# Kernel tuning notes

Measured on AMD Instinct MI355X. Metric: run time of the kernel, lower is better.

The kernel has to match this reference:

```python
import jax, jax.numpy as jnp
import numpy as np

N, K, P, C, H, E, Q, G = 50000, 8, 512, 64, 128, 1600000, 500000, 64

def _gelu(x):
    return jax.nn.gelu(x, approximate=False)  # torch F.gelu default = exact erf

def _mlp(x, Wi, bi, Wh, bh, Wo, bo, Wp=None, bp=None):
    # MLP: lin_in -> gelu -> hid -> (proj skip if in>hidden) -> skip+gelu -> lin_out
    skip = x if Wp is None else x @ Wp.T + bp
    h = _gelu(x @ Wi.T + bi)
    h = h @ Wh.T + bh
    return (skip + _gelu(h)) @ Wo.T + bo

def _sage(x, src, dst, Wl, bl, Wr, n):
    # PyG SAGEConv: mean-aggregate source features at dst, then lin_l(agg)+lin_r(x)
    s = jax.ops.segment_sum(x[src], dst, num_segments=n)
    cnt = jax.ops.segment_sum(jnp.ones((src.shape[0], 1), x.dtype), dst, num_segments=n)
    agg = s / jnp.maximum(cnt, 1.0)
    return agg @ Wl.T + bl + x @ Wr.T

def setup_inputs():
    key = jax.random.key(0)
    ks = iter(jax.random.split(key, 64))
    def lin(o, i):
        return (jax.random.normal(next(ks), (o, i), jnp.float32) / np.sqrt(i)).astype(jnp.float32)
    def bias(o):
        return jnp.zeros((o,), jnp.float32)
    inp = {}
    inp["x"] = jax.random.normal(next(ks), (N, K, P), jnp.float32)
    inp["batch"] = jnp.sort(jax.random.randint(next(ks), (N,), 0, G))
    inp["edge_index"] = jax.random.randint(next(ks), (2, E), 0, N)
    inp["src_idx"] = jax.random.randint(next(ks), (Q,), 0, N)
    inp["dst_idx"] = jax.random.randint(next(ks), (Q,), 0, N)
    # Embedder.mlp : MLP(P, P, H) with proj (P > H)
    inp.update(em_in_W=lin(H, P), em_in_b=bias(H), em_hid_W=lin(H, H), em_hid_b=bias(H),
               em_out_W=lin(P, H), em_out_b=bias(P), em_proj_W=lin(H, P), em_proj_b=bias(H))
    # Embedder.rho : MLP(P, C, H) with proj
    inp.update(rho_in_W=lin(H, P), rho_in_b=bias(H), rho_hid_W=lin(H, H), rho_hid_b=bias(H),
               rho_out_W=lin(C, H), rho_out_b=bias(C), rho_proj_W=lin(H, P), rho_proj_b=bias(H))
    for i in (1, 2, 3):
        inp[f"c{i}_ll_W"] = lin(C, C); inp[f"c{i}_ll_b"] = bias(C); inp[f"c{i}_lr_W"] = lin(C, C)
    # head MLP(3C, 2C, 2C) with proj (3C > 2C)
    inp.update(h1_in_W=lin(H, 3 * C), h1_in_b=bias(H), h1_hid_W=lin(H, H), h1_hid_b=bias(H),
               h1_out_W=lin(2 * C, H), h1_out_b=bias(2 * C), h1_proj_W=lin(H, 3 * C), h1_proj_b=bias(H))
    # head MLP(2C, 1, 2C), no proj
    inp.update(h2_in_W=lin(H, 2 * C), h2_in_b=bias(H), h2_hid_W=lin(H, H), h2_hid_b=bias(H),
               h2_out_W=lin(1, H), h2_out_b=bias(1))
    return inp

def reference(x, batch, edge_index, src_idx, dst_idx,
              em_in_W, em_in_b, em_hid_W, em_hid_b, em_out_W, em_out_b, em_proj_W, em_proj_b,
              rho_in_W, rho_in_b, rho_hid_W, rho_hid_b, rho_out_W, rho_out_b, rho_proj_W, rho_proj_b,
              c1_ll_W, c1_ll_b, c1_lr_W, c2_ll_W, c2_ll_b, c2_lr_W, c3_ll_W, c3_ll_b, c3_lr_W,
              h1_in_W, h1_in_b, h1_hid_W, h1_hid_b, h1_out_W, h1_out_b, h1_proj_W, h1_proj_b,
              h2_in_W, h2_in_b, h2_hid_W, h2_hid_b, h2_out_W, h2_out_b):
    n = x.shape[0]
    # Embedder: per-point MLP, gelu, sum over point-set dim, then rho (dropout = eval identity)
    h = _gelu(_mlp(x, em_in_W, em_in_b, em_hid_W, em_hid_b, em_out_W, em_out_b, em_proj_W, em_proj_b))
    z = _mlp(h.sum(-2), rho_in_W, rho_in_b, rho_hid_W, rho_hid_b, rho_out_W, rho_out_b, rho_proj_W, rho_proj_b)
    src, dst = edge_index[0], edge_index[1]
    z = z + _gelu(_sage(z, src, dst, c1_ll_W, c1_ll_b, c1_lr_W, n))
    z = z + _gelu(_sage(z, src, dst, c2_ll_W, c2_ll_b, c2_lr_W, n))
    z = z + _gelu(_sage(z, src, dst, c3_ll_W, c3_ll_b, c3_lr_W, n))
    node_embeddings = z
    # global_max_pool keyed by batch id, broadcast back via gather
    graph_emb = jax.ops.segment_max(z, batch, num_segments=G)
    ge = graph_emb[batch[src_idx]]  # == graph_emb[batch][src_idx]
    se, de = z[src_idx], z[dst_idx]
    xy = jnp.concatenate([se, de, ge], axis=-1)
    yx = jnp.concatenate([de, se, ge], axis=-1)
    def head(q):
        t = jax.nn.relu(_mlp(q, h1_in_W, h1_in_b, h1_hid_W, h1_hid_b, h1_out_W, h1_out_b, h1_proj_W, h1_proj_b))
        return _mlp(t, h2_in_W, h2_in_b, h2_hid_W, h2_hid_b, h2_out_W, h2_out_b)
    return (node_embeddings, (head(xy), head(yx)), xy)
```

## Files before the change

### kernel.cpp

```cpp
#include <hip/hip_runtime.h>

typedef unsigned short US;
typedef unsigned int   UI;
typedef short  short8 __attribute__((ext_vector_type(8)));
typedef US     u16x8  __attribute__((ext_vector_type(8)));
typedef float  f32x4  __attribute__((ext_vector_type(4)));

#define DEVI __device__ __forceinline__

DEVI float bf2f(US u){ UI i = ((UI)u) << 16; float f; __builtin_memcpy(&f, &i, 4); return f; }
DEVI US f2bf(float x){ UI i; __builtin_memcpy(&i, &x, 4); UI r = (i + 0x7FFFu + ((i >> 16) & 1u)) >> 16; return (US)r; }
DEVI float gelu_f(float x){
    float x2 = x * x;
    float m  = x * fmaf(x2, -0.1029432f, -2.3022052f);
    float e  = __builtin_amdgcn_exp2f(m);
    return x * __builtin_amdgcn_rcpf(1.0f + e);
}
DEVI UI encf(float f){ UI u; __builtin_memcpy(&u, &f, 4); return (u & 0x80000000u) ? ~u : (u | 0x80000000u); }
DEVI float decf(UI u){ UI b = (u & 0x80000000u) ? (u ^ 0x80000000u) : ~u; float f; __builtin_memcpy(&f, &b, 4); return f; }
DEVI int swz(int r, int c, int ld){ int i = r * ld + c; return i ^ ((r & 7) << 3); }

DEVI UI pkbf(float a, float b){ UI u; asm("v_cvt_pk_bf16_f32 %0, %1, %2" : "=v"(u) : "v"(a), "v"(b)); return u; }
DEVI void st4(US* T, int row, int col, float v0, float v1, float v2, float v3){
    uint2 p; p.x = pkbf(v0, v1); p.y = pkbf(v2, v3);
    *(uint2*)&T[swz(row, col, 256)] = p;
}
DEVI void ld4(const US* T, int row, int col, float& v0, float& v1, float& v2, float& v3){
    uint2 q = *(const uint2*)&T[swz(row, col, 256)];
    v0 = bf2f((US)(q.x & 0xffff)); v1 = bf2f((US)(q.x >> 16));
    v2 = bf2f((US)(q.y & 0xffff)); v3 = bf2f((US)(q.y >> 16));
}

enum : int { O_EmW1 = 0, O_EmWh = 131072, O_EmWo = 147456, O_RhoW1 = 212992,
             O_RhoWh = 344064, O_RhoWo = 360448, O_Cat1 = 368640, O_Cat2 = 376832,
             O_Cat3 = 385024, O_H1W1 = 393216, O_H1Wh = 442368, O_H1Wo = 458752,
             O_H2W1 = 475136, O_H2Wh = 491520, W_TOTAL = 507904 };

template<int NT, int NKC, int NTHR, bool SWAP = false>
DEVI void stageWD(const US* __restrict__ Wg, int Kw, const US* __restrict__ A, int lda,
                  int ab0, int ab1, int ab2, int arow0, US* Wb, int tid, f32x4 (&acc)[NT])
{
    const int lane = tid & 63;
    const int wc = (tid >> 6) & 1;
    constexpr int SLAB = NT * 32 * 64;
    #pragma unroll
    for (int n = 0; n < NT; ++n) acc[n] = (f32x4){0.f, 0.f, 0.f, 0.f};
    constexpr int J = (NT * 256) / NTHR;
    u16x8 wreg[J];
    #pragma unroll
    for (int j = 0; j < J; ++j) {
        const int c = tid + NTHR * j;
        wreg[j] = *(const u16x8*)(Wg + (size_t)(c >> 3) * Kw + (c & 7) * 8);
    }
    #pragma unroll
    for (int j = 0; j < J; ++j) {
        const int c = tid + NTHR * j;
        *(u16x8*)&Wb[swz(c >> 3, (c & 7) * 8, 64)] = wreg[j];
    }
    #pragma unroll
    for (int kc = 0; kc < NKC; ++kc) {
        __syncthreads();
        if (kc + 1 < NKC) {
            #pragma unroll
            for (int j = 0; j < J; ++j) {
                const int c = tid + NTHR * j;
                wreg[j] = *(const u16x8*)(Wg + (size_t)(c >> 3) * Kw + (kc + 1) * 64 + (c & 7) * 8);
            }
        }
        const int ab = (kc == 0) ? ab0 : ((kc == 1) ? ab1 : ab2);
        const int bufr = (kc & 1) * SLAB;
        #pragma unroll
        for (int sub = 0; sub < 2; ++sub) {
            const int kk = sub * 32 + ((lane >> 4) << 3);
            short8 a = *(const short8*)&A[swz(arow0 + (lane & 15), ab + kk, lda)];
            #pragma unroll
            for (int n = 0; n < NT; ++n) {
                short8 b = *(const short8*)&Wb[bufr + swz(wc * (NT * 16) + n * 16 + (lane & 15), kk, 64)];
                if (SWAP) acc[n] = __builtin_amdgcn_mfma_f32_16x16x32_bf16(b, a, acc[n], 0, 0, 0);
                else      acc[n] = __builtin_amdgcn_mfma_f32_16x16x32_bf16(a, b, acc[n], 0, 0, 0);
            }
        }
        if (kc + 1 < NKC) {
            const int bufw = ((kc + 1) & 1) * SLAB;
            #pragma unroll
            for (int j = 0; j < J; ++j) {
                const int c = tid + NTHR * j;
                *(u16x8*)&Wb[bufw + swz(c >> 3, (c & 7) * 8, 64)] = wreg[j];
            }
        }
    }
    __syncthreads();
}

template<int NT, int NTN, int NKC, int NTHR, bool LAST, bool SWAP = true>
DEVI void stageWC(const US* __restrict__ Wg, int Kw, const US* __restrict__ nextWg, int nKw,
                  const US* __restrict__ A, int lda, int ab0, int ab1, int ab2, int arow0,
                  US* Wb, int off0, int off1, int wrN, int tid, f32x4 (&acc)[NT])
{
    const int lane = tid & 63;
    const int wc = (tid >> 6) & 1;
    #pragma unroll
    for (int n = 0; n < NT; ++n) acc[n] = (f32x4){0.f, 0.f, 0.f, 0.f};
    constexpr int J  = (NT  * 256) / NTHR;
    constexpr int JN = (NTN * 256) / NTHR;
    constexpr int JM = (J > JN) ? J : JN;
    u16x8 wreg[JM];
    #pragma unroll
    for (int kc = 0; kc < NKC; ++kc) {
        __syncthreads();
        if (kc + 1 < NKC) {
            #pragma unroll
            for (int j = 0; j < J; ++j) {
                const int c = tid + NTHR * j;
                wreg[j] = *(const u16x8*)(Wg + (size_t)(c >> 3) * Kw + (kc + 1) * 64 + (c & 7) * 8);
            }
        } else if (!LAST) {
            #pragma unroll
            for (int j = 0; j < JN; ++j) {
                const int c = tid + NTHR * j;
                wreg[j] = *(const u16x8*)(nextWg + (size_t)(c >> 3) * nKw + (c & 7) * 8);
            }
        }
        const int ab = (kc == 0) ? ab0 : ((kc == 1) ? ab1 : ab2);
        const int rd = (kc & 1) ? off1 : off0;
        #pragma unroll
        for (int sub = 0; sub < 2; ++sub) {
            const int kk = sub * 32 + ((lane >> 4) << 3);
            short8 a = *(const short8*)&A[swz(arow0 + (lane & 15), ab + kk, lda)];
            #pragma unroll
            for (int n = 0; n < NT; ++n) {
                short8 b = *(const short8*)&Wb[rd + swz(wc * (NT * 16) + n * 16 + (lane & 15), kk, 64)];
                if (SWAP) acc[n] = __builtin_amdgcn_mfma_f32_16x16x32_bf16(b, a, acc[n], 0, 0, 0);
                else      acc[n] = __builtin_amdgcn_mfma_f32_16x16x32_bf16(a, b, acc[n], 0, 0, 0);
            }
        }
        if (kc + 1 < NKC) {
            const int wr_ = (kc & 1) ? off0 : off1;
            #pragma unroll
            for (int j = 0; j < J; ++j) {
                const int c = tid + NTHR * j;
                *(u16x8*)&Wb[wr_ + swz(c >> 3, (c & 7) * 8, 64)] = wreg[j];
            }
        } else if (!LAST) {
            #pragma unroll
            for (int j = 0; j < JN; ++j) {
                const int c = tid + NTHR * j;
                *(u16x8*)&Wb[wrN + swz(c >> 3, (c & 7) * 8, 64)] = wreg[j];
            }
        }
    }
    __syncthreads();
}

template<int NT, int NTHR>
DEVI void preloadW(const US* __restrict__ Wg, int Kw, US* Wb, int off, int tid)
{
    constexpr int J = (NT * 256) / NTHR;
    #pragma unroll
    for (int j = 0; j < J; ++j) {
        const int c = tid + NTHR * j;
        u16x8 v = *(const u16x8*)(Wg + (size_t)(c >> 3) * Kw + (c & 7) * 8);
        *(u16x8*)&Wb[off + swz(c >> 3, (c & 7) * 8, 64)] = v;
    }
}

__global__ __launch_bounds__(1024, 4)
void embed_fused(const float* __restrict__ x, const US* __restrict__ WB,
                 const float* __restrict__ b_in, const float* __restrict__ b_proj,
                 const float* __restrict__ b_hid, const float* __restrict__ b_out,
                 US* __restrict__ Ss)
{
    __shared__ __align__(16) US T1[128 * 256];
    __shared__ __align__(16) US Wb[2 * 16384];
    const int tid = threadIdx.x, lane = tid & 63, w = tid >> 6;
    const int wr = w >> 1, wc = w & 1;
    const int h = lane >> 4;
    const int grow0 = blockIdx.x * 128;
    const int rowT = wr * 16 + (lane & 15);

    {
        f32x4 acc[8];
        #pragma unroll
        for (int n = 0; n < 8; ++n) acc[n] = (f32x4){0.f, 0.f, 0.f, 0.f};
        const float* xp = x + (size_t)(grow0 + rowT) * 512 + h * 8;
        float4 pA0, pA1, pA2, pA3, pB0, pB1, pB2, pB3;
        u16x8 wreg[2];
        auto loadW = [&](int kc) {
            #pragma unroll
            for (int j = 0; j < 2; ++j) {
                const int c = tid + 1024 * j;
                wreg[j] = *(const u16x8*)(WB + O_EmW1 + (size_t)(c >> 3) * 512 + kc * 64 + (c & 7) * 8);
            }
        };
        auto writeW = [&](int buf) {
            #pragma unroll
            for (int j = 0; j < 2; ++j) {
                const int c = tid + 1024 * j;
                *(u16x8*)&Wb[buf * 16384 + swz(c >> 3, (c & 7) * 8, 64)] = wreg[j];
            }
        };
        pA0 = *(const float4*)(xp +   0); pA1 = *(const float4*)(xp +   4);
        pA2 = *(const float4*)(xp +  32); pA3 = *(const float4*)(xp +  36);
        loadW(0);
        pB0 = *(const float4*)(xp +  64); pB1 = *(const float4*)(xp +  68);
        pB2 = *(const float4*)(xp +  96); pB3 = *(const float4*)(xp + 100);
        writeW(0);
        #pragma unroll
        for (int k2 = 0; k2 < 4; ++k2) {
            const int kce = 2 * k2, kco = 2 * k2 + 1;
            __syncthreads();
            short8 a0, a1;
            {
                uint4 q;
                q.x = pkbf(pA0.x, pA0.y); q.y = pkbf(pA0.z, pA0.w);
                q.z = pkbf(pA1.x, pA1.y); q.w = pkbf(pA1.z, pA1.w);
                __builtin_memcpy(&a0, &q, 16);
                q.x = pkbf(pA2.x, pA2.y); q.y = pkbf(pA2.z, pA2.w);
                q.z = pkbf(pA3.x, pA3.y); q.w = pkbf(pA3.z, pA3.w);
                __builtin_memcpy(&a1, &q, 16);
            }
            if (kce + 2 < 8) {
                pA0 = *(const float4*)(xp + (kce + 2) * 64);
                pA1 = *(const float4*)(xp + (kce + 2) * 64 + 4);
                pA2 = *(const float4*)(xp + (kce + 2) * 64 + 32);
                pA3 = *(const float4*)(xp + (kce + 2) * 64 + 36);
            }
            loadW(kco);
            #pragma unroll
            for (int n = 0; n < 8; ++n) {
                short8 b = *(const short8*)&Wb[swz(wc * 128 + n * 16 + (lane & 15), h * 8, 64)];
                acc[n] = __builtin_amdgcn_mfma_f32_16x16x32_bf16(b, a0, acc[n], 0, 0, 0);
            }
            #pragma unroll
            for (int n = 0; n < 8; ++n) {
                short8 b = *(const short8*)&Wb[swz(wc * 128 + n * 16 + (lane & 15), 32 + h * 8, 64)];
                acc[n] = __builtin_amdgcn_mfma_f32_16x16x32_bf16(b, a1, acc[n], 0, 0, 0);
            }
            writeW(1);
            __syncthreads();
            {
                uint4 q;
                q.x = pkbf(pB0.x, pB0.y); q.y = pkbf(pB0.z, pB0.w);
                q.z = pkbf(pB1.x, pB1.y); q.w = pkbf(pB1.z, pB1.w);
                __builtin_memcpy(&a0, &q, 16);
                q.x = pkbf(pB2.x, pB2.y); q.y = pkbf(pB2.z, pB2.w);
                q.z = pkbf(pB3.x, pB3.y); q.w = pkbf(pB3.z, pB3.w);
                __builtin_memcpy(&a1, &q, 16);
            }
            if (kco + 2 < 8) {
                pB0 = *(const float4*)(xp + (kco + 2) * 64);
                pB1 = *(const float4*)(xp + (kco + 2) * 64 + 4);
                pB2 = *(const float4*)(xp + (kco + 2) * 64 + 32);
                pB3 = *(const float4*)(xp + (kco + 2) * 64 + 36);
            }
            u16x8 nx;
            if (kco < 7) loadW(kco + 1);
            else         nx = *(const u16x8*)(WB + O_EmWh + (size_t)(tid >> 3) * 128 + (tid & 7) * 8);
            #pragma unroll
            for (int n = 0; n < 8; ++n) {
                short8 b = *(const short8*)&Wb[16384 + swz(wc * 128 + n * 16 + (lane & 15), h * 8, 64)];
                acc[n] = __builtin_amdgcn_mfma_f32_16x16x32_bf16(b, a0, acc[n], 0, 0, 0);
            }
            #pragma unroll
            for (int n = 0; n < 8; ++n) {
                short8 b = *(const short8*)&Wb[16384 + swz(wc * 128 + n * 16 + (lane & 15), 32 + h * 8, 64)];
                acc[n] = __builtin_amdgcn_mfma_f32_16x16x32_bf16(b, a1, acc[n], 0, 0, 0);
            }
            if (kco < 7) writeW(0);
            else         *(u16x8*)&Wb[swz(tid >> 3, (tid & 7) * 8, 64)] = nx;
        }
        #pragma unroll
        for (int n = 0; n < 8; ++n) {
            const int col = wc * 128 + n * 16 + h * 4;
            float4 bv = (col < 128) ? *(const float4*)&b_in[col]
                                    : *(const float4*)&b_proj[col - 128];
            float v0 = acc[n][0] + bv.x, v1 = acc[n][1] + bv.y;
            float v2 = acc[n][2] + bv.z, v3 = acc[n][3] + bv.w;
            if (col < 128) { v0 = gelu_f(v0); v1 = gelu_f(v1); v2 = gelu_f(v2); v3 = gelu_f(v3); }
            st4(T1, rowT, col, v0, v1, v2, v3);
        }
    }
    {
        f32x4 acc[4];
        stageWC<4, 8, 2, 1024, false, true>(WB + O_EmWh, 128, WB + O_EmWo, 128,
                                            T1, 256, 0, 64, 0, wr * 16,
                                            Wb, 0, 8192, 16384, tid, acc);
        #pragma unroll
        for (int n = 0; n < 4; ++n) {
            const int col = wc * 64 + n * 16 + h * 4;
            float4 bv = *(const float4*)&b_hid[col];
            float s0, s1, s2, s3;
            ld4(T1, rowT, 128 + col, s0, s1, s2, s3);
            st4(T1, rowT, col,
                gelu_f(acc[n][0] + bv.x) + s0, gelu_f(acc[n][1] + bv.y) + s1,
                gelu_f(acc[n][2] + bv.z) + s2, gelu_f(acc[n][3] + bv.w) + s3);
        }
    }
    {
        f32x4 acc[8];
        stageWC<8, 8, 2, 1024, false, false>(WB + O_EmWo, 128, WB + O_EmWo + (size_t)256 * 128, 128,
                                             T1, 256, 0, 64, 0, wr * 16,
                                             Wb, 16384, 0, 16384, tid, acc);
        #pragma unroll
        for (int n = 0; n < 8; ++n) {
            const int col = wc * 128 + n * 16 + (lane & 15);
            const float bv = b_out[col];
            float s = 0.f;
            #pragma unroll
            for (int r = 0; r < 4; ++r) s += gelu_f(acc[n][r] + bv);
            s += __shfl_xor(s, 16);
            if (((lane >> 4) & 1) == 0) {
                const int node = (grow0 >> 3) + wr * 2 + (lane >> 5);
                Ss[(size_t)node * 512 + col] = f2bf(s);
            }
        }
    }
    {
        f32x4 acc[8];
        stageWC<8, 8, 2, 1024, true, false>(WB + O_EmWo + (size_t)256 * 128, 128, (const US*)nullptr, 0,
                                            T1, 256, 0, 64, 0, wr * 16,
                                            Wb, 16384, 0, 16384, tid, acc);
        #pragma unroll
        for (int n = 0; n < 8; ++n) {
            const int col = wc * 128 + n * 16 + (lane & 15);
            const float bv = b_out[256 + col];
            float s = 0.f;
            #pragma unroll
            for (int r = 0; r < 4; ++r) s += gelu_f(acc[n][r] + bv);
            s += __shfl_xor(s, 16);
            if (((lane >> 4) & 1) == 0) {
                const int node = (grow0 >> 3) + wr * 2 + (lane >> 5);
                Ss[(size_t)node * 512 + 256 + col] = f2bf(s);
            }
        }
    }
}

__global__ __launch_bounds__(512, 2)
void rho_fused(const US* __restrict__ Ss, const US* __restrict__ WB,
               const float* __restrict__ b_in, const float* __restrict__ b_proj,
               const float* __restrict__ b_hid, const float* __restrict__ b_out,
               US* __restrict__ zo, int N)
{
    __shared__ __align__(16) US T1[64 * 256];
    __shared__ __align__(16) US Wb[256 * 64];
    const int tid = threadIdx.x, lane = tid & 63, w = tid >> 6;
    const int wr = w >> 1, wc = w & 1;
    const int h = lane >> 4;
    const int grow0 = blockIdx.x * 64;
    const int rowT = wr * 16 + (lane & 15);

    {
        f32x4 acc[8];
        #pragma unroll
        for (int n = 0; n < 8; ++n) acc[n] = (f32x4){0.f, 0.f, 0.f, 0.f};
        int arow = grow0 + rowT; if (arow >= N) arow = N - 1;
        const US* sp = Ss + (size_t)arow * 512 + h * 8;
        u16x8 a0r, a1r, wreg[4];
        auto loadA = [&](int kc) {
            a0r = *(const u16x8*)(sp + kc * 64);
            a1r = *(const u16x8*)(sp + kc * 64 + 32);
        };
        auto loadW = [&](int kc) {
            #pragma unroll
            for (int j = 0; j < 4; ++j) {
                const int c = tid + 512 * j;
                wreg[j] = *(const u16x8*)(WB + O_RhoW1 + (size_t)(c >> 3) * 512 + kc * 64 + (c & 7) * 8);
            }
        };
        loadA(0); loadW(0);
        for (int kc = 0; kc < 8; ++kc) {
            __syncthreads();
            #pragma unroll
            for (int j = 0; j < 4; ++j) {
                const int c = tid + 512 * j;
                *(u16x8*)&Wb[swz(c >> 3, (c & 7) * 8, 64)] = wreg[j];
            }
            __syncthreads();
            if (kc < 7) loadW(kc + 1);
            short8 a0, a1;
            __builtin_memcpy(&a0, &a0r, 16);
            __builtin_memcpy(&a1, &a1r, 16);
            #pragma unroll
            for (int n = 0; n < 8; ++n) {
                short8 b = *(const short8*)&Wb[swz(wc * 128 + n * 16 + (lane & 15), h * 8, 64)];
                acc[n] = __builtin_amdgcn_mfma_f32_16x16x32_bf16(b, a0, acc[n], 0, 0, 0);
            }
            #pragma unroll
            for (int n = 0; n < 8; ++n) {
                short8 b = *(const short8*)&Wb[swz(wc * 128 + n * 16 + (lane & 15), 32 + h * 8, 64)];
                acc[n] = __builtin_amdgcn_mfma_f32_16x16x32_bf16(b, a1, acc[n], 0, 0, 0);
            }
            if (kc < 7) loadA(kc + 1);
        }
        __syncthreads();
        #pragma unroll
        for (int n = 0; n < 8; ++n) {
            const int col = wc * 128 + n * 16 + h * 4;
            float4 bv = (col < 128) ? *(const float4*)&b_in[col]
                                    : *(const float4*)&b_proj[col - 128];
            float v0 = acc[n][0] + bv.x, v1 = acc[n][1] + bv.y;
            float v2 = acc[n][2] + bv.z, v3 = acc[n][3] + bv.w;
            if (col < 128) { v0 = gelu_f(v0); v1 = gelu_f(v1); v2 = gelu_f(v2); v3 = gelu_f(v3); }
            st4(T1, rowT, col, v0, v1, v2, v3);
        }
    }
    {
        f32x4 acc[4];
        stageWD<4, 2, 512, true>(WB + O_RhoWh, 128, T1, 256, 0, 64, 0, wr * 16, Wb, tid, acc);
        #pragma unroll
        for (int n = 0; n < 4; ++n) {
            const int col = wc * 64 + n * 16 + h * 4;
            float4 bv = *(const float4*)&b_hid[col];
            float s0, s1, s2, s3;
            ld4(T1, rowT, 128 + col, s0, s1, s2, s3);
            st4(T1, rowT, col,
                gelu_f(acc[n][0] + bv.x) + s0, gelu_f(acc[n][1] + bv.y) + s1,
                gelu_f(acc[n][2] + bv.z) + s2, gelu_f(acc[n][3] + bv.w) + s3);
        }
    }
    {
        f32x4 acc[2];
        stageWD<2, 2, 512>(WB + O_RhoWo, 128, T1, 256, 0, 64, 0, wr * 16, Wb, tid, acc);
        #pragma unroll
        for (int n = 0; n < 2; ++n) {
            const int col = wc * 32 + n * 16 + (lane & 15);
            const float bv = b_out[col];
            #pragma unroll
            for (int r = 0; r < 4; ++r) {
                const int node = grow0 + wr * 16 + h * 4 + r;
                if (node < N) zo[(size_t)node * 64 + col] = f2bf(acc[n][r] + bv);
            }
        }
    }
}

__global__ __launch_bounds__(1024, 4)
void head_fused(const int* __restrict__ srcq, const int* __restrict__ dstq,
                const int* __restrict__ batch, const US* __restrict__ z,
                const US* __restrict__ geb, const US* __restrict__ WB,
                const float* __restrict__ b1_in, const float* __restrict__ b1_proj,
                const float* __restrict__ b1_hid, const float* __restrict__ b1_out,
                const float* __restrict__ b2_in, const float* __restrict__ b2_hid,
                const float* __restrict__ w2_out, const float* __restrict__ b2_out,
                float* __restrict__ outH, float* __restrict__ outXY, int Q)
{
    __shared__ __align__(16) US A0[64 * 192];
    __shared__ __align__(16) US T1[128 * 256];
    __shared__ __align__(16) US Wb[2 * 16384];
    __shared__ float wout_s[128];
    const int tid = threadIdx.x, lane = tid & 63, w = tid >> 6;
    const int wr = w >> 1, wc = w & 1;
    const int q0 = blockIdx.x * 64;
    const int s1a = (wr < 4) ? 0 : 64;
    const int s1b = (wr < 4) ? 64 : 0;
    const int arowS1 = (wr & 3) * 16;
    const int rowS1 = (wr >> 2) * 64 + arowS1 + (lane & 15);
    const int rowT  = wr * 16 + (lane & 15);

    preloadW<8, 1024>(WB + O_H1W1, 192, Wb, 0, tid);

    {
        if (tid < 512) {
            const int r = tid >> 3, hh = tid & 7;
            const int q = q0 + r;
            const int qc = (q < Q) ? q : (Q - 1);
            const int s = srcq[qc], d = dstq[qc];
            const int g = batch[s];
            *(u16x8*)&A0[swz(r, hh * 8, 192)]       = *(const u16x8*)(z + (size_t)s * 64 + hh * 8);
            *(u16x8*)&A0[swz(r, 64 + hh * 8, 192)]  = *(const u16x8*)(z + (size_t)d * 64 + hh * 8);
            *(u16x8*)&A0[swz(r, 128 + hh * 8, 192)] = *(const u16x8*)(geb + (size_t)g * 64 + hh * 8);
        }
        if (tid < 128) wout_s[tid] = w2_out[tid];
    }
    __syncthreads();
    {
        const int row = tid >> 4;
        const int qu  = tid & 15;
        #pragma unroll
        for (int jj = 0; jj < 3; ++jj) {
            const int c4 = (jj * 16 + qu) * 4;
            if (q0 + row < Q) {
                const US* p = &A0[swz(row, c4, 192)];
                float4 o;
                o.x = bf2f(p[0]); o.y = bf2f(p[1]); o.z = bf2f(p[2]); o.w = bf2f(p[3]);
                *(float4*)&outXY[(size_t)(q0 + row) * 192 + c4] = o;
            }
        }
    }
    {
        f32x4 acc8[8];
        stageWC<8, 4, 3, 1024, false>(WB + O_H1W1, 192, WB + O_H1Wh, 128,
                                      A0, 192, s1a, s1b, 128, arowS1,
                                      Wb, 0, 16384, 16384, tid, acc8);
        #pragma unroll
        for (int n = 0; n < 8; ++n) {
            const int col = wc * 128 + n * 16 + ((lane >> 4) << 2);
            float4 bv = (col < 128) ? *(const float4*)&b1_in[col]
                                    : *(const float4*)&b1_proj[col - 128];
            float v0 = acc8[n][0] + bv.x, v1 = acc8[n][1] + bv.y;
            float v2 = acc8[n][2] + bv.z, v3 = acc8[n][3] + bv.w;
            if (col < 128) { v0 = gelu_f(v0); v1 = gelu_f(v1); v2 = gelu_f(v2); v3 = gelu_f(v3); }
            st4(T1, rowS1, col, v0, v1, v2, v3);
        }
    }
    f32x4 acc[4];
    stageWC<4, 4, 2, 1024, false>(WB + O_H1Wh, 128, WB + O_H1Wo, 128,
                                  T1, 256, 0, 64, 0, wr * 16,
                                  Wb, 16384, 24576, 16384, tid, acc);
    #pragma unroll
    for (int n = 0; n < 4; ++n) {
        const int col = wc * 64 + n * 16 + ((lane >> 4) << 2);
        float4 bv = *(const float4*)&b1_hid[col];
        float s0, s1, s2, s3;
        ld4(T1, rowT, 128 + col, s0, s1, s2, s3);
        st4(T1, rowT, col,
            gelu_f(acc[n][0] + bv.x) + s0, gelu_f(acc[n][1] + bv.y) + s1,
            gelu_f(acc[n][2] + bv.z) + s2, gelu_f(acc[n][3] + bv.w) + s3);
    }
    stageWC<4, 4, 2, 1024, false>(WB + O_H1Wo, 128, WB + O_H2W1, 128,
                                  T1, 256, 0, 64, 0, wr * 16,
                                  Wb, 16384, 24576, 16384, tid, acc);
    #pragma unroll
    for (int n = 0; n < 4; ++n) {
        const int col = wc * 64 + n * 16 + ((lane >> 4) << 2);
        float4 bv = *(const float4*)&b1_out[col];
        st4(T1, rowT, 128 + col,
            fmaxf(acc[n][0] + bv.x, 0.f), fmaxf(acc[n][1] + bv.y, 0.f),
            fmaxf(acc[n][2] + bv.z, 0.f), fmaxf(acc[n][3] + bv.w, 0.f));
    }
    stageWC<4, 4, 2, 1024, false>(WB + O_H2W1, 128, WB + O_H2Wh, 128,
                                  T1, 256, 128, 192, 0, wr * 16,
                                  Wb, 16384, 24576, 16384, tid, acc);
    #pragma unroll
    for (int n = 0; n < 4; ++n) {
        const int col = wc * 64 + n * 16 + ((lane >> 4) << 2);
        float4 bv = *(const float4*)&b2_in[col];
        st4(T1, rowT, col,
            gelu_f(acc[n][0] + bv.x), gelu_f(acc[n][1] + bv.y),
            gelu_f(acc[n][2] + bv.z), gelu_f(acc[n][3] + bv.w));
    }
    stageWC<4, 4, 2, 1024, true>(WB + O_H2Wh, 128, (const US*)nullptr, 0,
                                 T1, 256, 0, 64, 0, wr * 16,
                                 Wb, 16384, 24576, 16384, tid, acc);
    #pragma unroll
    for (int n = 0; n < 4; ++n) {
        const int col = wc * 64 + n * 16 + ((lane >> 4) << 2);
        float4 bv = *(const float4*)&b2_hid[col];
        float t0, t1, t2, t3;
        ld4(T1, rowT, 128 + col, t0, t1, t2, t3);
        st4(T1, rowT, col,
            gelu_f(acc[n][0] + bv.x) + t0, gelu_f(acc[n][1] + bv.y) + t1,
            gelu_f(acc[n][2] + bv.z) + t2, gelu_f(acc[n][3] + bv.w) + t3);
    }
    __syncthreads();
    {
        const int r = tid >> 3, hh = tid & 7;
        float a = 0.f;
        u16x8 v0 = *(const u16x8*)&T1[swz(r, hh * 16, 256)];
        u16x8 v1 = *(const u16x8*)&T1[swz(r, hh * 16 + 8, 256)];
        #pragma unroll
        for (int e = 0; e < 8; ++e) {
            a += bf2f(v0[e]) * wout_s[hh * 16 + e];
            a += bf2f(v1[e]) * wout_s[hh * 16 + 8 + e];
        }
        a += __shfl_xor(a, 4);
        a += __shfl_xor(a, 2);
        a += __shfl_xor(a, 1);
        const int q = q0 + (r & 63);
        if ((lane & 7) == 0 && q < Q) outH[(size_t)(r >> 6) * Q + q] = a + b2_out[0];
    }
}

__global__ __launch_bounds__(256, 2)
void sage_gemm(const US* __restrict__ zin, const US* __restrict__ agg,
               const US* __restrict__ Wc, const float* __restrict__ bias,
               US* __restrict__ zout, float* __restrict__ fout, int N)
{
    __shared__ __align__(16) US As[128 * 128];
    __shared__ __align__(16) US Ws[64 * 128];
    const int tid = threadIdx.x, lane = tid & 63, w = tid >> 6;
    const int grow0 = blockIdx.x * 128;
    {
        const int r = tid >> 1, hh = tid & 1;
        int row = grow0 + r; if (row >= N) row = N - 1;
        const US* src = hh ? (zin + (size_t)row * 64) : (agg + (size_t)row * 64);
        #pragma unroll
        for (int j = 0; j < 8; ++j)
            *(u16x8*)&As[swz(r, hh * 64 + 8 * j, 128)] = *(const u16x8*)(src + 8 * j);
    }
    #pragma unroll
    for (int j = 0; j < 4; ++j) {
        const int c = tid + 256 * j;
        *(u16x8*)&Ws[swz(c >> 4, (c & 15) * 8, 128)] =
            *(const u16x8*)(Wc + (size_t)(c >> 4) * 128 + (c & 15) * 8);
    }
    __syncthreads();
    const int rbw = w * 32;
    f32x4 acc[2][4];
    #pragma unroll
    for (int m = 0; m < 2; ++m)
        #pragma unroll
        for (int n = 0; n < 4; ++n) acc[m][n] = (f32x4){0.f, 0.f, 0.f, 0.f};
    #pragma unroll
    for (int kc = 0; kc < 2; ++kc)
        #pragma unroll
        for (int sub = 0; sub < 2; ++sub) {
            const int kk = kc * 64 + sub * 32 + ((lane >> 4) << 3);
            short8 a[2], b[4];
            #pragma unroll
            for (int m = 0; m < 2; ++m) a[m] = *(const short8*)&As[swz(rbw + m * 16 + (lane & 15), kk, 128)];
            #pragma unroll
            for (int n = 0; n < 4; ++n) b[n] = *(const short8*)&Ws[swz(n * 16 + (lane & 15), kk, 128)];
            #pragma unroll
            for (int m = 0; m < 2; ++m)
                #pragma unroll
                for (int n = 0; n < 4; ++n)
                    acc[m][n] = __builtin_amdgcn_mfma_f32_16x16x32_bf16(a[m], b[n], acc[m][n], 0, 0, 0);
        }
    #pragma unroll
    for (int m = 0; m < 2; ++m) {
        const int row0 = rbw + m * 16 + ((lane >> 4) << 2);
        #pragma unroll
        for (int n = 0; n < 4; ++n) {
            const int col = n * 16 + (lane & 15);
            const float bv = bias[col];
            #pragma unroll
            for (int r = 0; r < 4; ++r) {
                const int node = grow0 + row0 + r;
                if (node < N) {
                    const float v = gelu_f(acc[m][n][r] + bv) + bf2f(zin[(size_t)node * 64 + col]);
                    const US bb = f2bf(v);
                    zout[(size_t)node * 64 + col] = bb;
                    if (fout) fout[(size_t)node * 64 + col] = bf2f(bb);
                }
            }
        }
    }
}

struct WSeg { const float* src; int dst; int n; int rl; int ldd; };
struct WPrm { WSeg s[20]; };

__global__ void prep_w(WPrm p, US* __restrict__ wb)
{
    WSeg sg = p.s[blockIdx.x];
    for (int i = threadIdx.x; i < sg.n; i += 256) {
        const int idx = sg.dst + (i / sg.rl) * sg.ldd + (i % sg.rl);
        wb[idx] = f2bf(sg.src[i]);
    }
}

__global__ void count_k(const int* __restrict__ dst, int* __restrict__ cnt, int E)
{
    int e = blockIdx.x * 256 + threadIdx.x;
    if (e < E) atomicAdd(&cnt[dst[e]], 1);
}

__global__ void scan_csr(const int* __restrict__ cnt, int n, int* __restrict__ indp, int* __restrict__ curs)
{
    __shared__ int wsum[16];
    __shared__ int carry_s;
    const int tid = threadIdx.x, lane = tid & 63, w = tid >> 6;
    if (tid == 0) carry_s = 0;
    __syncthreads();
    for (int base = 0; base < n; base += 1024) {
        const int i = base + tid;
        const int v = (i < n) ? cnt[i] : 0;
        int s = v;
        #pragma unroll
        for (int o = 1; o < 64; o <<= 1) { int t = __shfl_up(s, o); if (lane >= o) s += t; }
        if (lane == 63) wsum[w] = s;
        __syncthreads();
        if (w == 0 && lane < 16) {
            int ws2 = wsum[lane];
            #pragma unroll
            for (int o = 1; o < 16; o <<= 1) { int t = __shfl_up(ws2, o); if (lane >= o) ws2 += t; }
            wsum[lane] = ws2;
        }
        __syncthreads();
        const int carry = carry_s;
        const int woff  = (w == 0) ? 0 : wsum[w - 1];
        if (i < n) { const int excl = carry + woff + s - v; indp[i] = excl; curs[i] = excl; }
        __syncthreads();
        if (tid == 0) carry_s = carry + wsum[15];
        __syncthreads();
    }
    if (threadIdx.x == 0) indp[n] = carry_s;
}

__global__ void fill_k(const int* __restrict__ src, const int* __restrict__ dst,
                       int* __restrict__ curs, int* __restrict__ esrc, int E)
{
    int e = blockIdx.x * 256 + threadIdx.x;
    if (e < E) { int p = atomicAdd(&curs[dst[e]], 1); esrc[p] = src[e]; }
}

__global__ void sage_agg(const US* __restrict__ z, const int* __restrict__ indp,
                         const int* __restrict__ esrc, US* __restrict__ agg, int n)
{
    const int w = blockIdx.x * 4 + (threadIdx.x >> 6);
    const int lane = threadIdx.x & 63;
    if (w >= n) return;
    const int beg = indp[w], end = indp[w + 1];
    float acc = 0.f;
    int j = beg;
    for (; j + 4 <= end; j += 4) {
        const int s0 = esrc[j], s1 = esrc[j + 1], s2 = esrc[j + 2], s3 = esrc[j + 3];
        const float v0 = bf2f(z[(size_t)s0 * 64 + lane]);
        const float v1 = bf2f(z[(size_t)s1 * 64 + lane]);
        const float v2 = bf2f(z[(size_t)s2 * 64 + lane]);
        const float v3 = bf2f(z[(size_t)s3 * 64 + lane]);
        acc += (v0 + v1) + (v2 + v3);
    }
    for (; j < end; ++j) acc += bf2f(z[(size_t)esrc[j] * 64 + lane]);
    const float d = (float)(end - beg);
    agg[(size_t)w * 64 + lane] = f2bf(acc / fmaxf(d, 1.0f));
}

__global__ void segmax_k(const US* __restrict__ z, const int* __restrict__ batch,
                         UI* __restrict__ enc, int n, int per)
{
    const int w = blockIdx.x * 4 + (threadIdx.x >> 6);
    const int lane = threadIdx.x & 63;
    const int start = w * per;
    if (start >= n) return;
    const int end = (start + per < n) ? start + per : n;
    int g = batch[start];
    float m = -3.0e38f;
    for (int i = start; i < end; ++i) {
        const int b = batch[i];
        if (b != g) { atomicMax(&enc[(size_t)g * 64 + lane], encf(m)); g = b; m = -3.0e38f; }
        m = fmaxf(m, bf2f(z[(size_t)i * 64 + lane]));
    }
    atomicMax(&enc[(size_t)g * 64 + lane], encf(m));
}

__global__ void decode_ge(const UI* __restrict__ enc, US* __restrict__ geb)
{
    const int i = blockIdx.x * 256 + threadIdx.x;
    if (i < 4096) geb[i] = f2bf(decf(enc[i]));
}

extern "C" void kernel_launch(void* const* d_in, const int* in_sizes, int n_in,
                              void* d_out, int out_size, void* d_ws, size_t ws_size,
                              hipStream_t stream)
{
    (void)in_sizes; (void)n_in; (void)out_size; (void)ws_size;

    const float* x      = (const float*)d_in[0];
    const int*   batch  = (const int*)d_in[1];
    const int*   eidx   = (const int*)d_in[2];
    const int*   srcq   = (const int*)d_in[3];
    const int*   dstq   = (const int*)d_in[4];
    const float* em_in_b   = (const float*)d_in[6];
    const float* em_hid_b  = (const float*)d_in[8];
    const float* em_out_b  = (const float*)d_in[10];
    const float* em_proj_b = (const float*)d_in[12];
    const float* rho_in_b  = (const float*)d_in[14];
    const float* rho_hid_b = (const float*)d_in[16];
    const float* rho_out_b = (const float*)d_in[18];
    const float* rho_proj_b= (const float*)d_in[20];
    const float* c_ll_W[3] = {(const float*)d_in[21], (const float*)d_in[24], (const float*)d_in[27]};
    const float* c_ll_b[3] = {(const float*)d_in[22], (const float*)d_in[25], (const float*)d_in[28]};
    const float* c_lr_W[3] = {(const float*)d_in[23], (const float*)d_in[26], (const float*)d_in[29]};
    const float* h1_in_b   = (const float*)d_in[31];
    const float* h1_hid_b  = (const float*)d_in[33];
    const float* h1_out_b  = (const float*)d_in[35];
    const float* h1_proj_b = (const float*)d_in[37];
    const float* h2_in_b   = (const float*)d_in[39];
    const float* h2_hid_b  = (const float*)d_in[41];
    const float* h2_out_W  = (const float*)d_in[42];
    const float* h2_out_b  = (const float*)d_in[43];

    const int N = 50000, E = 1600000, Q = 500000;
    float* out = (float*)d_out;

    char* wsb = (char*)d_ws;
    size_t off = 0;
    auto ALLOC = [&](size_t bytes) -> char* {
        char* p = wsb + off; off = (off + bytes + 255) & ~(size_t)255; return p;
    };
    US*  WB   = (US*)ALLOC((size_t)W_TOTAL * 2);
    US*  Ss   = (US*)ALLOC((size_t)N * 512 * 2);
    US*  z0   = (US*)ALLOC((size_t)N * 64 * 2);
    US*  z1   = (US*)ALLOC((size_t)N * 64 * 2);
    US*  aggB = (US*)ALLOC((size_t)N * 64 * 2);
    int* cnt  = (int*)ALLOC((size_t)N * 4);
    int* indp = (int*)ALLOC((size_t)(N + 1) * 4);
    int* curs = (int*)ALLOC((size_t)N * 4);
    int* esrc = (int*)ALLOC((size_t)E * 4);
    UI*  enc  = (UI*)ALLOC(4096 * 4);
    US*  geb  = (US*)ALLOC(4096 * 2);

    const int catOff[3] = {O_Cat1, O_Cat2, O_Cat3};

    WPrm pw; int si = 0;
    auto SEG = [&](const float* s, int o, int n, int rl, int ldd) {
        pw.s[si].src = s; pw.s[si].dst = o; pw.s[si].n = n; pw.s[si].rl = rl; pw.s[si].ldd = ldd; ++si;
    };
    SEG((const float*)d_in[5],  O_EmW1,          65536, 65536, 65536);
    SEG((const float*)d_in[11], O_EmW1 + 65536,  65536, 65536, 65536);
    SEG((const float*)d_in[7],  O_EmWh,          16384, 16384, 16384);
    SEG((const float*)d_in[9],  O_EmWo,          65536, 65536, 65536);
    SEG((const float*)d_in[13], O_RhoW1,         65536, 65536, 65536);
    SEG((const float*)d_in[19], O_RhoW1 + 65536, 65536, 65536, 65536);
    SEG((const float*)d_in[15], O_RhoWh,         16384, 16384, 16384);
    SEG((const float*)d_in[17], O_RhoWo,          8192,  8192,  8192);
    for (int i = 0; i < 3; ++i) {
        SEG(c_ll_W[i], catOff[i],      4096, 64, 128);
        SEG(c_lr_W[i], catOff[i] + 64, 4096, 64, 128);
    }
    SEG((const float*)d_in[30], O_H1W1,          24576, 24576, 24576);
    SEG((const float*)d_in[36], O_H1W1 + 24576,  24576, 24576, 24576);
    SEG((const float*)d_in[32], O_H1Wh,          16384, 16384, 16384);
    SEG((const float*)d_in[34], O_H1Wo,          16384, 16384, 16384);
    SEG((const float*)d_in[38], O_H2W1,          16384, 16384, 16384);
    SEG((const float*)d_in[40], O_H2Wh,          16384, 16384, 16384);
    prep_w<<<dim3(20), dim3(256), 0, stream>>>(pw, WB);

    hipMemsetAsync(cnt, 0, (size_t)N * 4, stream);
    count_k<<<dim3((E + 255) / 256), dim3(256), 0, stream>>>(eidx + E, cnt, E);
    scan_csr<<<dim3(1), dim3(1024), 0, stream>>>(cnt, N, indp, curs);
    fill_k<<<dim3((E + 255) / 256), dim3(256), 0, stream>>>(eidx, eidx + E, curs, esrc, E);

    embed_fused<<<dim3(3125), dim3(1024), 0, stream>>>(x, WB, em_in_b, em_proj_b, em_hid_b, em_out_b, Ss);
    rho_fused<<<dim3((N + 63) / 64), dim3(512), 0, stream>>>(Ss, WB, rho_in_b, rho_proj_b, rho_hid_b, rho_out_b, z0, N);

    US* zin = z0; US* zout = z1;
    for (int ci = 0; ci < 3; ++ci) {
        sage_agg<<<dim3((N + 3) / 4), dim3(256), 0, stream>>>(zin, indp, esrc, aggB, N);
        sage_gemm<<<dim3((N + 127) / 128), dim3(256), 0, stream>>>(
            zin, aggB, WB + catOff[ci], c_ll_b[ci], zout,
            (ci == 2) ? out : (float*)nullptr, N);
        US* t = zin; zin = zout; zout = t;
    }
    US* zf = zin;

    hipMemsetAsync(enc, 0, 4096 * 4, stream);
    segmax_k<<<dim3((N + 511) / 512), dim3(256), 0, stream>>>(zf, batch, enc, N, 128);
    decode_ge<<<dim3(16), dim3(256), 0, stream>>>(enc, geb);

    head_fused<<<dim3((Q + 63) / 64), dim3(1024), 0, stream>>>(
        srcq, dstq, batch, zf, geb, WB,
        h1_in_b, h1_proj_b, h1_hid_b, h1_out_b, h2_in_b, h2_hid_b, h2_out_W, h2_out_b,
        out + (size_t)N * 64, out + (size_t)N * 64 + 2 * (size_t)Q, Q);
}
```

Measured before the change: 1.544 ms.

## Retile MLP stages so each wave computes two row tiles sharing weight fragments

Replaces the per-wave 16-row × wide-column GEMM tiling with a 4×4 warp grid where each wave processes two 16-row tiles (rows r and r+64) over a narrower column slice. Each weight fragment read from LDS now feeds two MFMAs, which roughly halves LDS traffic for the B operand across the embedder tail and head MLP stages. The cost is an extra A-fragment load and doubled accumulators per wave, which raises register pressure under the 1024-thread launch bound.

```diff
diff --git a/kernel.cpp b/kernel.cpp
--- a/kernel.cpp
+++ b/kernel.cpp
@@ -92,17 +92,24 @@
     __syncthreads();
 }
 
-template<int NT, int NTN, int NKC, int NTHR, bool LAST, bool SWAP = true>
-DEVI void stageWC(const US* __restrict__ Wg, int Kw, const US* __restrict__ nextWg, int nKw,
-                  const US* __restrict__ A, int lda, int ab0, int ab1, int ab2, int arow0,
-                  US* Wb, int off0, int off1, int wrN, int tid, f32x4 (&acc)[NT])
+template<int NT, int TOTC, int TOTCN, int NKC, bool LAST, bool SWAP>
+DEVI void stageWC2(const US* __restrict__ Wg, int Kw, const US* __restrict__ nextWg, int nKw,
+                   const US* __restrict__ A, int lda,
+                   int aA0, int aA1, int aA2, int aB0, int aB1, int aB2,
+                   int arowA, int rofB, int colb,
+                   US* Wb, int off0, int off1, int wrN, int tid,
+                   f32x4 (&accA)[NT], f32x4 (&accB)[NT])
 {
     const int lane = tid & 63;
-    const int wc = (tid >> 6) & 1;
-    #pragma unroll
-    for (int n = 0; n < NT; ++n) acc[n] = (f32x4){0.f, 0.f, 0.f, 0.f};
-    constexpr int J  = (NT  * 256) / NTHR;
-    constexpr int JN = (NTN * 256) / NTHR;
+    const int l15 = lane & 15;
+    const int h8 = (lane >> 4) << 3;
+    #pragma unroll
+    for (int n = 0; n < NT; ++n) {
+        accA[n] = (f32x4){0.f, 0.f, 0.f, 0.f};
+        accB[n] = (f32x4){0.f, 0.f, 0.f, 0.f};
+    }
+    constexpr int J  = TOTC  / 128;
+    constexpr int JN = TOTCN / 128;
     constexpr int JM = (J > JN) ? J : JN;
     u16x8 wreg[JM];
     #pragma unroll
@@ -111,40 +118,47 @@
         if (kc + 1 < NKC) {
             #pragma unroll
             for (int j = 0; j < J; ++j) {
-                const int c = tid + NTHR * j;
+                const int c = tid + 1024 * j;
                 wreg[j] = *(const u16x8*)(Wg + (size_t)(c >> 3) * Kw + (kc + 1) * 64 + (c & 7) * 8);
             }
         } else if (!LAST) {
             #pragma unroll
             for (int j = 0; j < JN; ++j) {
-                const int c = tid + NTHR * j;
+                const int c = tid + 1024 * j;
                 wreg[j] = *(const u16x8*)(nextWg + (size_t)(c >> 3) * nKw + (c & 7) * 8);
             }
         }
-        const int ab = (kc == 0) ? ab0 : ((kc == 1) ? ab1 : ab2);
+        const int abA = (kc == 0) ? aA0 : ((kc == 1) ? aA1 : aA2);
+        const int abB = (kc == 0) ? aB0 : ((kc == 1) ? aB1 : aB2);
         const int rd = (kc & 1) ? off1 : off0;
         #pragma unroll
         for (int sub = 0; sub < 2; ++sub) {
-            const int kk = sub * 32 + ((lane >> 4) << 3);
-            short8 a = *(const short8*)&A[swz(arow0 + (lane & 15), ab + kk, lda)];
+            const int kk = sub * 32 + h8;
+            short8 aA = *(const short8*)&A[swz(arowA + l15, abA + kk, lda)];
+            short8 aB = *(const short8*)&A[swz(arowA + rofB + l15, abB + kk, lda)];
             #pragma unroll
             for (int n = 0; n < NT; ++n) {
-                short8 b = *(const short8*)&Wb[rd + swz(wc * (NT * 16) + n * 16 + (lane & 15), kk, 64)];
-                if (SWAP) acc[n] = __builtin_amdgcn_mfma_f32_16x16x32_bf16(b, a, acc[n], 0, 0, 0);
-                else      acc[n] = __builtin_amdgcn_mfma_f32_16x16x32_bf16(a, b, acc[n], 0, 0, 0);
+                short8 b = *(const short8*)&Wb[rd + swz(colb + n * 16 + l15, kk, 64)];
+                if (SWAP) {
+                    accA[n] = __builtin_amdgcn_mfma_f32_16x16x32_bf16(b, aA, accA[n], 0, 0, 0);
+                    accB[n] = __builtin_amdgcn_mfma_f32_16x16x32_bf16(b, aB, accB[n], 0, 0, 0);
+                } else {
+                    accA[n] = __builtin_amdgcn_mfma_f32_16x16x32_bf16(aA, b, accA[n], 0, 0, 0);
+                    accB[n] = __builtin_amdgcn_mfma_f32_16x16x32_bf16(aB, b, accB[n], 0, 0, 0);
+                }
             }
         }
         if (kc + 1 < NKC) {
             const int wr_ = (kc & 1) ? off0 : off1;
             #pragma unroll
             for (int j = 0; j < J; ++j) {
-                const int c = tid + NTHR * j;
+                const int c = tid + 1024 * j;
                 *(u16x8*)&Wb[wr_ + swz(c >> 3, (c & 7) * 8, 64)] = wreg[j];
             }
         } else if (!LAST) {
             #pragma unroll
             for (int j = 0; j < JN; ++j) {
-                const int c = tid + NTHR * j;
+                const int c = tid + 1024 * j;
                 *(u16x8*)&Wb[wrN + swz(c >> 3, (c & 7) * 8, 64)] = wreg[j];
             }
         }
@@ -175,8 +189,12 @@
     const int tid = threadIdx.x, lane = tid & 63, w = tid >> 6;
     const int wr = w >> 1, wc = w & 1;
     const int h = lane >> 4;
+    const int l15 = lane & 15;
     const int grow0 = blockIdx.x * 128;
-    const int rowT = wr * 16 + (lane & 15);
+    const int rowT = wr * 16 + l15;
+    const int wr4 = w & 3, cq = w >> 2;
+    const int arowA = wr4 * 16;
+    const int rA = arowA + l15, rB = rA + 64;
 
     {
         f32x4 acc[8];
@@ -228,12 +246,12 @@
             loadW(kco);
             #pragma unroll
             for (int n = 0; n < 8; ++n) {
-                short8 b = *(const short8*)&Wb[swz(wc * 128 + n * 16 + (lane & 15), h * 8, 64)];
+                short8 b = *(const short8*)&Wb[swz(wc * 128 + n * 16 + l15, h * 8, 64)];
                 acc[n] = __builtin_amdgcn_mfma_f32_16x16x32_bf16(b, a0, acc[n], 0, 0, 0);
             }
             #pragma unroll
             for (int n = 0; n < 8; ++n) {
-                short8 b = *(const short8*)&Wb[swz(wc * 128 + n * 16 + (lane & 15), 32 + h * 8, 64)];
+                short8 b = *(const short8*)&Wb[swz(wc * 128 + n * 16 + l15, 32 + h * 8, 64)];
                 acc[n] = __builtin_amdgcn_mfma_f32_16x16x32_bf16(b, a1, acc[n], 0, 0, 0);
             }
             writeW(1);
@@ -258,12 +276,12 @@
             else         nx = *(const u16x8*)(WB + O_EmWh + (size_t)(tid >> 3) * 128 + (tid & 7) * 8);
             #pragma unroll
             for (int n = 0; n < 8; ++n) {
-                short8 b = *(const short8*)&Wb[16384 + swz(wc * 128 + n * 16 + (lane & 15), h * 8, 64)];
+                short8 b = *(const short8*)&Wb[16384 + swz(wc * 128 + n * 16 + l15, h * 8, 64)];
                 acc[n] = __builtin_amdgcn_mfma_f32_16x16x32_bf16(b, a0, acc[n], 0, 0, 0);
             }
             #pragma unroll
             for (int n = 0; n < 8; ++n) {
-                short8 b = *(const short8*)&Wb[16384 + swz(wc * 128 + n * 16 + (lane & 15), 32 + h * 8, 64)];
+                short8 b = *(const short8*)&Wb[16384 + swz(wc * 128 + n * 16 + l15, 32 + h * 8, 64)];
                 acc[n] = __builtin_amdgcn_mfma_f32_16x16x32_bf16(b, a1, acc[n], 0, 0, 0);
             }
             if (kco < 7) writeW(0);
@@ -281,56 +299,52 @@
         }
     }
     {
-        f32x4 acc[4];
-        stageWC<4, 8, 2, 1024, false, true>(WB + O_EmWh, 128, WB + O_EmWo, 128,
-                                            T1, 256, 0, 64, 0, wr * 16,
-                                            Wb, 0, 8192, 16384, tid, acc);
-        #pragma unroll
-        for (int n = 0; n < 4; ++n) {
-            const int col = wc * 64 + n * 16 + h * 4;
+        f32x4 accA[2], accB[2];
+        stageWC2<2, 128, 256, 2, false, true>(WB + O_EmWh, 128, WB + O_EmWo, 128,
+                                              T1, 256, 0, 64, 0, 0, 64, 0,
+                                              arowA, 64, cq * 32,
+                                              Wb, 0, 8192, 16384, tid, accA, accB);
+        #pragma unroll
+        for (int n = 0; n < 2; ++n) {
+            const int col = cq * 32 + n * 16 + h * 4;
             float4 bv = *(const float4*)&b_hid[col];
             float s0, s1, s2, s3;
-            ld4(T1, rowT, 128 + col, s0, s1, s2, s3);
-            st4(T1, rowT, col,
-                gelu_f(acc[n][0] + bv.x) + s0, gelu_f(acc[n][1] + bv.y) + s1,
-                gelu_f(acc[n][2] + bv.z) + s2, gelu_f(acc[n][3] + bv.w) + s3);
-        }
-    }
-    {
-        f32x4 acc[8];
-        stageWC<8, 8, 2, 1024, false, false>(WB + O_EmWo, 128, WB + O_EmWo + (size_t)256 * 128, 128,
-                                             T1, 256, 0, 64, 0, wr * 16,
-                                             Wb, 16384, 0, 16384, tid, acc);
-        #pragma unroll
-        for (int n = 0; n < 8; ++n) {
-            const int col = wc * 128 + n * 16 + (lane & 15);
-            const float bv = b_out[col];
-            float s = 0.f;
-            #pragma unroll
-            for (int r = 0; r < 4; ++r) s += gelu_f(acc[n][r] + bv);
-            s += __shfl_xor(s, 16);
+            ld4(T1, rA, 128 + col, s0, s1, s2, s3);
+            st4(T1, rA, col,
+                gelu_f(accA[n][0] + bv.x) + s0, gelu_f(accA[n][1] + bv.y) + s1,
+                gelu_f(accA[n][2] + bv.z) + s2, gelu_f(accA[n][3] + bv.w) + s3);
+            ld4(T1, rB, 128 + col, s0, s1, s2, s3);
+            st4(T1, rB, col,
+                gelu_f(accB[n][0] + bv.x) + s0, gelu_f(accB[n][1] + bv.y) + s1,
+                gelu_f(accB[n][2] + bv.z) + s2, gelu_f(accB[n][3] + bv.w) + s3);
+        }
+    }
+    #pragma unroll
+    for (int p2 = 0; p2 < 2; ++p2) {
+        f32x4 accA[4], accB[4];
+        if (p2 == 0)
+            stageWC2<4, 256, 256, 2, false, false>(WB + O_EmWo, 128, WB + O_EmWo + (size_t)256 * 128, 128,
+                                                   T1, 256, 0, 64, 0, 0, 64, 0,
+                                                   arowA, 64, cq * 64,
+                                                   Wb, 16384, 0, 16384, tid, accA, accB);
+        else
+            stageWC2<4, 256, 256, 2, true, false>(WB + O_EmWo + (size_t)256 * 128, 128, (const US*)nullptr, 0,
+                                                  T1, 256, 0, 64, 0, 0, 64, 0,
+                                                  arowA, 64, cq * 64,
+                                                  Wb, 16384, 0, 16384, tid, accA, accB);
+        #pragma unroll
+        for (int n = 0; n < 4; ++n) {
+            const int col = cq * 64 + n * 16 + l15;
+            const float bv = b_out[p2 * 256 + col];
+            float sA = 0.f, sB = 0.f;
+            #pragma unroll
+            for (int r = 0; r < 4; ++r) { sA += gelu_f(accA[n][r] + bv); sB += gelu_f(accB[n][r] + bv); }
+            sA += __shfl_xor(sA, 16);
+            sB += __shfl_xor(sB, 16);
             if (((lane >> 4) & 1) == 0) {
-                const int node = (grow0 >> 3) + wr * 2 + (lane >> 5);
-                Ss[(size_t)node * 512 + col] = f2bf(s);
-            }
-        }
-    }
-    {
-        f32x4 acc[8];
-        stageWC<8, 8, 2, 1024, true, false>(WB + O_EmWo + (size_t)256 * 128, 128, (const US*)nullptr, 0,
-                                            T1, 256, 0, 64, 0, wr * 16,
-                                            Wb, 16384, 0, 16384, tid, acc);
-        #pragma unroll
-        for (int n = 0; n < 8; ++n) {
-            const int col = wc * 128 + n * 16 + (lane & 15);
-            const float bv = b_out[256 + col];
-            float s = 0.f;
-            #pragma unroll
-            for (int r = 0; r < 4; ++r) s += gelu_f(acc[n][r] + bv);
-            s += __shfl_xor(s, 16);
-            if (((lane >> 4) & 1) == 0) {
-                const int node = (grow0 >> 3) + wr * 2 + (lane >> 5);
-                Ss[(size_t)node * 512 + 256 + col] = f2bf(s);
+                const int nodeA = (grow0 >> 3) + wr4 * 2 + (lane >> 5);
+                Ss[(size_t)nodeA * 512 + p2 * 256 + col] = f2bf(sA);
+                Ss[(size_t)(nodeA + 8) * 512 + p2 * 256 + col] = f2bf(sB);
             }
         }
     }
@@ -450,13 +464,12 @@
     __shared__ __align__(16) US Wb[2 * 16384];
     __shared__ float wout_s[128];
     const int tid = threadIdx.x, lane = tid & 63, w = tid >> 6;
-    const int wr = w >> 1, wc = w & 1;
+    const int l15 = lane & 15;
+    const int h4 = (lane >> 4) << 2;
     const int q0 = blockIdx.x * 64;
-    const int s1a = (wr < 4) ? 0 : 64;
-    const int s1b = (wr < 4) ? 64 : 0;
-    const int arowS1 = (wr & 3) * 16;
-    const int rowS1 = (wr >> 2) * 64 + arowS1 + (lane & 15);
-    const int rowT  = wr * 16 + (lane & 15);
+    const int wr4 = w & 3, cq = w >> 2;
+    const int arowA = wr4 * 16;
+    const int rA = arowA + l15, rB = rA + 64;
 
     preloadW<8, 1024>(WB + O_H1W1, 192, Wb, 0, tid);
 
@@ -489,69 +502,95 @@
         }
     }
     {
-        f32x4 acc8[8];
-        stageWC<8, 4, 3, 1024, false>(WB + O_H1W1, 192, WB + O_H1Wh, 128,
-                                      A0, 192, s1a, s1b, 128, arowS1,
-                                      Wb, 0, 16384, 16384, tid, acc8);
-        #pragma unroll
-        for (int n = 0; n < 8; ++n) {
-            const int col = wc * 128 + n * 16 + ((lane >> 4) << 2);
+        f32x4 accA[4], accB[4];
+        stageWC2<4, 256, 128, 3, false, true>(WB + O_H1W1, 192, WB + O_H1Wh, 128,
+                                              A0, 192, 0, 64, 128, 64, 0, 128,
+                                              arowA, 0, cq * 64,
+                                              Wb, 0, 16384, 16384, tid, accA, accB);
+        #pragma unroll
+        for (int n = 0; n < 4; ++n) {
+            const int col = cq * 64 + n * 16 + h4;
             float4 bv = (col < 128) ? *(const float4*)&b1_in[col]
                                     : *(const float4*)&b1_proj[col - 128];
-            float v0 = acc8[n][0] + bv.x, v1 = acc8[n][1] + bv.y;
-            float v2 = acc8[n][2] + bv.z, v3 = acc8[n][3] + bv.w;
-            if (col < 128) { v0 = gelu_f(v0); v1 = gelu_f(v1); v2 = gelu_f(v2); v3 = gelu_f(v3); }
-            st4(T1, rowS1, col, v0, v1, v2, v3);
-        }
-    }
-    f32x4 acc[4];
-    stageWC<4, 4, 2, 1024, false>(WB + O_H1Wh, 128, WB + O_H1Wo, 128,
-                                  T1, 256, 0, 64, 0, wr * 16,
-                                  Wb, 16384, 24576, 16384, tid, acc);
-    #pragma unroll
-    for (int n = 0; n < 4; ++n) {
-        const int col = wc * 64 + n * 16 + ((lane >> 4) << 2);
+            float v0 = accA[n][0] + bv.x, v1 = accA[n][1] + bv.y;
+            float v2 = accA[n][2] + bv.z, v3 = accA[n][3] + bv.w;
+            float u0 = accB[n][0] + bv.x, u1 = accB[n][1] + bv.y;
+            float u2 = accB[n][2] + bv.z, u3 = accB[n][3] + bv.w;
+            if (col < 128) {
+                v0 = gelu_f(v0); v1 = gelu_f(v1); v2 = gelu_f(v2); v3 = gelu_f(v3);
+                u0 = gelu_f(u0); u1 = gelu_f(u1); u2 = gelu_f(u2); u3 = gelu_f(u3);
+            }
+            st4(T1, rA, col, v0, v1, v2, v3);
+            st4(T1, rB, col, u0, u1, u2, u3);
+        }
+    }
+    f32x4 accA[2], accB[2];
+    const int colb2 = cq * 32;
+    stageWC2<2, 128, 128, 2, false, true>(WB + O_H1Wh, 128, WB + O_H1Wo, 128,
+                                          T1, 256, 0, 64, 0, 0, 64, 0,
+                                          arowA, 64, colb2,
+                                          Wb, 16384, 24576, 16384, tid, accA, accB);
+    #pragma unroll
+    for (int n = 0; n < 2; ++n) {
+        const int col = colb2 + n * 16 + h4;
         float4 bv = *(const float4*)&b1_hid[col];
         float s0, s1, s2, s3;
-        ld4(T1, rowT, 128 + col, s0, s1, s2, s3);
-        st4(T1, rowT, col,
-            gelu_f(acc[n][0] + bv.x) + s0, gelu_f(acc[n][1] + bv.y) + s1,
-            gelu_f(acc[n][2] + bv.z) + s2, gelu_f(acc[n][3] + bv.w) + s3);
-    }
-    stageWC<4, 4, 2, 1024, false>(WB + O_H1Wo, 128, WB + O_H2W1, 128,
-                                  T1, 256, 0, 64, 0, wr * 16,
-                                  Wb, 16384, 24576, 16384, tid, acc);
-    #pragma unroll
-    for (int n = 0; n < 4; ++n) {
-        const int col = wc * 64 + n * 16 + ((lane >> 4) << 2);
+        ld4(T1, rA, 128 + col, s0, s1, s2, s3);
+        st4(T1, rA, col,
+            gelu_f(accA[n][0] + bv.x) + s0, gelu_f(accA[n][1] + bv.y) + s1,
+            gelu_f(accA[n][2] + bv.z) + s2, gelu_f(accA[n][3] + bv.w) + s3);
+        ld4(T1, rB, 128 + col, s0, s1, s2, s3);
+        st4(T1, rB, col,
+            gelu_f(accB[n][0] + bv.x) + s0, gelu_f(accB[n][1] + bv.y) + s1,
+            gelu_f(accB[n][2] + bv.z) + s2, gelu_f(accB[n][3] + bv.w) + s3);
+    }
+    stageWC2<2, 128, 128, 2, false, true>(WB + O_H1Wo, 128, WB + O_H2W1, 128,
+                                          T1, 256, 0, 64, 0, 0, 64, 0,
+                                          arowA, 64, colb2,
+                                          Wb, 16384, 24576, 16384, tid, accA, accB);
+    #pragma unroll
+    for (int n = 0; n < 2; ++n) {
+        const int col = colb2 + n * 16 + h4;
         float4 bv = *(const float4*)&b1_out[col];
-        st4(T1, rowT, 128 + col,
-            fmaxf(acc[n][0] + bv.x, 0.f), fmaxf(acc[n][1] + bv.y, 0.f),
-            fmaxf(acc[n][2] + bv.z, 0.f), fmaxf(acc[n][3] + bv.w, 0.f));
-    }
-    stageWC<4, 4, 2, 1024, false>(WB + O_H2W1, 128, WB + O_H2Wh, 128,
-                                  T1, 256, 128, 192, 0, wr * 16,
-                                  Wb, 16384, 24576, 16384, tid, acc);
-    #pragma unroll
-    for (int n = 0; n < 4; ++n) {
-        const int col = wc * 64 + n * 16 + ((lane >> 4) << 2);
+        st4(T1, rA, 128 + col,
+            fmaxf(accA[n][0] + bv.x, 0.f), fmaxf(accA[n][1] + bv.y, 0.f),
+            fmaxf(accA[n][2] + bv.z, 0.f), fmaxf(accA[n][3] + bv.w, 0.f));
+        st4(T1, rB, 128 + col,
+            fmaxf(accB[n][0] + bv.x, 0.f), fmaxf(accB[n][1] + bv.y, 0.f),
+            fmaxf(accB[n][2] + bv.z, 0.f), fmaxf(accB[n][3] + bv.w, 0.f));
+    }
+    stageWC2<2, 128, 128, 2, false, true>(WB + O_H2W1, 128, WB + O_H2Wh, 128,
+                                          T1, 256, 128, 192, 0, 128, 192, 0,
+                                          arowA, 64, colb2,
+                                          Wb, 16384, 24576, 16384, tid, accA, accB);
+    #pragma unroll
+    for (int n = 0; n < 2; ++n) {
+        const int col = colb2 + n * 16 + h4;
         float4 bv = *(const float4*)&b2_in[col];
-        st4(T1, rowT, col,
-            gelu_f(acc[n][0] + bv.x), gelu_f(acc[n][1] + bv.y),
-            gelu_f(acc[n][2] + bv.z), gelu_f(acc[n][3] + bv.w));
-    }
-    stageWC<4, 4, 2, 1024, true>(WB + O_H2Wh, 128, (const US*)nullptr, 0,
-                                 T1, 256, 0, 64, 0, wr * 16,
-                                 Wb, 16384, 24576, 16384, tid, acc);
-    #pragma unroll
-    for (int n = 0; n < 4; ++n) {
-        const int col = wc * 64 + n * 16 + ((lane >> 4) << 2);
+        st4(T1, rA, col,
+            gelu_f(accA[n][0] + bv.x), gelu_f(accA[n][1] + bv.y),
+            gelu_f(accA[n][2] + bv.z), gelu_f(accA[n][3] + bv.w));
+        st4(T1, rB, col,
+            gelu_f(accB[n][0] + bv.x), gelu_f(accB[n][1] + bv.y),
+            gelu_f(accB[n][2] + bv.z), gelu_f(accB[n][3] + bv.w));
+    }
+    stageWC2<2, 128, 128, 2, true, true>(WB + O_H2Wh, 128, (const US*)nullptr, 0,
+                                         T1, 256, 0, 64, 0, 0, 64, 0,
+                                         arowA, 64, colb2,
+                                         Wb, 16384, 24576, 16384, tid, accA, accB);
+    #pragma unroll
+    for (int n = 0; n < 2; ++n) {
+        const int col = colb2 + n * 16 + h4;
         float4 bv = *(const float4*)&b2_hid[col];
         float t0, t1, t2, t3;
-        ld4(T1, rowT, 128 + col, t0, t1, t2, t3);
-        st4(T1, rowT, col,
-            gelu_f(acc[n][0] + bv.x) + t0, gelu_f(acc[n][1] + bv.y) + t1,
-            gelu_f(acc[n][2] + bv.z) + t2, gelu_f(acc[n][3] + bv.w) + t3);
+        ld4(T1, rA, 128 + col, t0, t1, t2, t3);
+        st4(T1, rA, col,
+            gelu_f(accA[n][0] + bv.x) + t0, gelu_f(accA[n][1] + bv.y) + t1,
+            gelu_f(accA[n][2] + bv.z) + t2, gelu_f(accA[n][3] + bv.w) + t3);
+        ld4(T1, rB, 128 + col, t0, t1, t2, t3);
+        st4(T1, rB, col,
+            gelu_f(accB[n][0] + bv.x) + t0, gelu_f(accB[n][1] + bv.y) + t1,
+            gelu_f(accB[n][2] + bv.z) + t2, gelu_f(accB[n][3] + bv.w) + t3);
     }
     __syncthreads();
     {
```

New measurement: 1.456 ms. 1.06x faster.
